# Performance work log

Hardware: AMD Instinct MI355X
Metric: run time of the kernel (lower is better)

## Reference

```python
import jax, jax.numpy as jnp
import numpy as np

NUM_NODES = 1_000_000
H_DIM = 64
OUT_DIM = 32
NUM_RELS = 64
NUM_BASES = 4
N_SRC0 = 400_000
N_DST1 = 100_000
N_DST2 = 20_000
E1 = 600_000
E2 = 300_000


def setup_inputs() -> dict:
    key = jax.random.key(0)
    ks = jax.random.split(key, 16)
    inp = {
        "input_nodes": jax.random.randint(ks[0], (N_SRC0,), 0, NUM_NODES),
        "src1": jax.random.randint(ks[1], (E1,), 0, N_SRC0),
        "dst1": jax.random.randint(ks[2], (E1,), 0, N_DST1),
        "etype1": jax.random.randint(ks[3], (E1,), 0, NUM_RELS),
        "norm1": jax.random.uniform(ks[4], (E1, 1), dtype=jnp.float32),
        "src2": jax.random.randint(ks[5], (E2,), 0, N_DST1),
        "dst2": jax.random.randint(ks[6], (E2,), 0, N_DST2),
        "etype2": jax.random.randint(ks[7], (E2,), 0, NUM_RELS),
        "norm2": jax.random.uniform(ks[8], (E2, 1), dtype=jnp.float32),
        # learned parameters
        "emb": jax.random.normal(ks[9], (NUM_NODES, H_DIM), dtype=jnp.float32),
        "V1": jax.random.normal(ks[10], (NUM_BASES, H_DIM, H_DIM), dtype=jnp.float32) * 0.05,
        "comp1": jax.random.normal(ks[11], (NUM_RELS, NUM_BASES), dtype=jnp.float32) * 0.3,
        "b1": jnp.zeros((H_DIM,), dtype=jnp.float32),
        "V2": jax.random.normal(ks[12], (NUM_BASES, H_DIM, OUT_DIM), dtype=jnp.float32) * 0.05,
        "comp2": jax.random.normal(ks[13], (NUM_RELS, NUM_BASES), dtype=jnp.float32) * 0.3,
        "b2": jnp.zeros((OUT_DIM,), dtype=jnp.float32),
    }
    return inp


def rel_graph_conv(x, src, dst, etype, norm, V, comp, bias, n_dst):
    """Basis-decomposed RelGraphConv (no self-loop): m_e = (x[src_e] @ W_{etype_e}) * norm_e,
    with W_r = sum_b comp[r,b] V[b]; aggregate by sum into dst nodes, then add bias."""
    xe = x[src]                                 # [E, d] gather of source features
    coeff = comp[etype]                         # [E, B] relation coefficients per edge
    y = jnp.einsum('ed,bdo->ebo', xe, V)        # [E, B, o] feature x each basis
    m = jnp.einsum('ebo,eb->eo', y, coeff)      # [E, o] relation-specific message
    m = m * norm                                # per-edge normalization ([E,1] broadcast)
    h = jax.ops.segment_sum(m, dst, num_segments=n_dst)  # scatter-add to dst
    return h + bias


def reference(input_nodes, src1, dst1, etype1, norm1, src2, dst2, etype2, norm2,
              emb, V1, comp1, b1, V2, comp2, b2):
    x = emb[input_nodes]                                           # [N_src0, h]
    h = rel_graph_conv(x, src1, dst1, etype1, norm1, V1, comp1, b1, N_DST1)
    h = jax.nn.relu(h)
    out = rel_graph_conv(h, src2, dst2, etype2, norm2, V2, comp2, b2, N_DST2)
    return out
```

## Files before the change

### kernel.cpp

```cpp
#include <hip/hip_runtime.h>
#include <stdint.h>

#define NUM_NODES 1000000
#define H_DIM 64
#define OUT_DIM 32
#define NUM_RELS 64
#define NUM_BASES 4
#define N_SRC0 400000
#define N_DST1 100000
#define N_DST2 20000
#define E1 600000
#define E2 300000
#define NDST_TOT (N_DST1 + N_DST2)
#define E_TOT (E1 + E2)

typedef __attribute__((ext_vector_type(8))) short bf16x8;
typedef __attribute__((ext_vector_type(4))) float floatx4;

__device__ __forceinline__ unsigned short f2bf(float f){
  union{float f; unsigned u;} v; v.f=f;
  unsigned u=v.u;
  unsigned r=(u + 0x7FFFu + ((u>>16)&1u))>>16;
  return (unsigned short)r;
}
__device__ __forceinline__ float bf2f(unsigned short h){
  union{unsigned u; float f;} v; v.u=((unsigned)h)<<16; return v.f;
}

__global__ void k_init(const float* __restrict__ V1, const float* __restrict__ V2,
                       ushort* __restrict__ Btab1, ushort* __restrict__ Btab2,
                       int* __restrict__ deg){
  int t = blockIdx.x*blockDim.x + threadIdx.x;
  if (t < NDST_TOT) deg[t] = 0;
  if (t < 16384){
    int j = t & 7, lane = (t>>3)&63, kk = (t>>9)&7, nt = t>>12;
    int kdim = kk*32 + (lane>>4)*8 + j;
    int o = nt*16 + (lane&15);
    int k = kdim>>2, b = kdim&3;
    Btab1[t] = f2bf(V1[(b*64 + k)*64 + o]);
  } else if (t < 24576){
    int u = t - 16384;
    int j = u & 7, lane = (u>>3)&63, kk = (u>>9)&7, nt = u>>12;
    int kdim = kk*32 + (lane>>4)*8 + j;
    int o = nt*16 + (lane&15);
    int k = kdim>>2, b = kdim&3;
    Btab2[u] = f2bf(V2[(b*64 + k)*32 + o]);
  }
}

__global__ void k_gather_x(const int* __restrict__ input_nodes,
                           const float* __restrict__ emb,
                           ushort* __restrict__ x_bf){
  int t = blockIdx.x*blockDim.x + threadIdx.x;
  if (t >= N_SRC0*16) return;
  int row = t >> 4, seg = t & 15;
  int idx = input_nodes[row];
  float4 v = ((const float4*)emb)[(size_t)idx*16 + seg];
  ushort4 o; o.x=f2bf(v.x); o.y=f2bf(v.y); o.z=f2bf(v.z); o.w=f2bf(v.w);
  ((ushort4*)x_bf)[(size_t)row*16 + seg] = o;
}

__global__ void k_hist(const int* __restrict__ dst1, const int* __restrict__ dst2,
                       int* __restrict__ deg){
  int t = blockIdx.x*blockDim.x + threadIdx.x;
  if (t < E1) atomicAdd(&deg[dst1[t]], 1);
  else if (t < E_TOT) atomicAdd(&deg[N_DST1 + dst2[t - E1]], 1);
}

__global__ void k_scan_sum(const int* __restrict__ deg, int* __restrict__ bsum, int n){
  __shared__ int lds[256];
  int tid = threadIdx.x;
  int base = blockIdx.x*1024 + tid*4;
  int s = 0;
  #pragma unroll
  for (int j=0;j<4;j++){ int i = base+j; if (i<n) s += deg[i]; }
  lds[tid] = s; __syncthreads();
  for (int off=128; off>0; off>>=1){ if (tid<off) lds[tid] += lds[tid+off]; __syncthreads(); }
  if (tid==0) bsum[blockIdx.x] = lds[0];
}

__global__ void k_scan_bsum(const int* __restrict__ bsum, int* __restrict__ boff, int nb){
  __shared__ int lds[256];
  int tid = threadIdx.x;
  int v = (tid<nb) ? bsum[tid] : 0;
  lds[tid] = v; __syncthreads();
  for (int off=1; off<256; off<<=1){
    int t = (tid>=off) ? lds[tid-off] : 0; __syncthreads();
    lds[tid] += t; __syncthreads();
  }
  if (tid<nb) boff[tid] = lds[tid] - v;
}

__global__ void k_scan_final(const int* __restrict__ deg, const int* __restrict__ boff,
                             int* __restrict__ offs, int* __restrict__ cursor, int n){
  __shared__ int lds[256];
  int tid = threadIdx.x;
  int base = blockIdx.x*1024 + tid*4;
  int a[4]; int s = 0;
  #pragma unroll
  for (int j=0;j<4;j++){ int i = base+j; a[j] = (i<n)?deg[i]:0; s += a[j]; }
  lds[tid] = s; __syncthreads();
  for (int off=1; off<256; off<<=1){
    int t = (tid>=off) ? lds[tid-off] : 0; __syncthreads();
    lds[tid] += t; __syncthreads();
  }
  int run = boff[blockIdx.x] + (lds[tid] - s);
  #pragma unroll
  for (int j=0;j<4;j++){
    int i = base+j;
    if (i<n){
      offs[i] = run; cursor[i] = run;
      run += a[j];
      if (i == n-1) offs[n] = run;
    }
  }
}

__global__ void k_scatter(const int* __restrict__ src1, const int* __restrict__ dst1,
                          const int* __restrict__ ety1, const float* __restrict__ nrm1,
                          const float* __restrict__ comp1,
                          const int* __restrict__ src2, const int* __restrict__ dst2,
                          const int* __restrict__ ety2, const float* __restrict__ nrm2,
                          const float* __restrict__ comp2,
                          int* __restrict__ cursor, int* __restrict__ ssrc,
                          float4* __restrict__ sc){
  int t = blockIdx.x*blockDim.x + threadIdx.x;
  int d, s, et; float nv; const float* comp;
  if (t < E1){
    d = dst1[t]; s = src1[t]; et = ety1[t]; nv = nrm1[t]; comp = comp1;
  } else if (t < E_TOT){
    int e = t - E1;
    d = N_DST1 + dst2[e]; s = src2[e]; et = ety2[e]; nv = nrm2[e]; comp = comp2;
  } else return;
  int p = atomicAdd(&cursor[d], 1);
  ssrc[p] = s;
  float4 cp = ((const float4*)comp)[et];
  float4 c; c.x = cp.x*nv; c.y = cp.y*nv; c.z = cp.z*nv; c.w = cp.w*nv;
  sc[p] = c;
}

__device__ __forceinline__ void agg_rows(const ushort* __restrict__ xin,
                                         const int* __restrict__ offs,
                                         const int* __restrict__ ssrc,
                                         const float4* __restrict__ sc,
                                         int mbase, int w, int lane,
                                         ushort zt[16][264]){
  for (int j = 0; j < 4; j++){
    int row = w*4 + j;
    int d = mbase + row;
    int e0 = offs[d], e1 = offs[d+1];
    float a0=0.f, a1=0.f, a2=0.f, a3=0.f;
    for (int base = e0; base < e1; base += 64){
      int m = e1 - base; if (m > 64) m = 64;
      int se = 0; float4 ce = {0.f,0.f,0.f,0.f};
      if (lane < m){ se = ssrc[base + lane]; ce = sc[base + lane]; }
      for (int i = 0; i < m; i++){
        int s = __shfl(se, i);
        float cx = __shfl(ce.x, i), cy = __shfl(ce.y, i);
        float cz = __shfl(ce.z, i), cw = __shfl(ce.w, i);
        float xv = bf2f(xin[(size_t)s*64 + lane]);
        a0 = fmaf(cx, xv, a0); a1 = fmaf(cy, xv, a1);
        a2 = fmaf(cz, xv, a2); a3 = fmaf(cw, xv, a3);
      }
    }
    ushort4 o; o.x=f2bf(a0); o.y=f2bf(a1); o.z=f2bf(a2); o.w=f2bf(a3);
    *(ushort4*)&zt[row][lane*4] = o;
  }
}

__global__ __launch_bounds__(256) void k_agg_gemm1(
    const ushort* __restrict__ xin, const int* __restrict__ offs,
    const int* __restrict__ ssrc, const float4* __restrict__ sc,
    const ushort* __restrict__ Btab, const float* __restrict__ bias,
    ushort* __restrict__ h_bf){
  __shared__ ushort zt[16][264];
  int lane = threadIdx.x & 63;
  int w = threadIdx.x >> 6;
  int mbase = blockIdx.x * 16;
  agg_rows(xin, offs, ssrc, sc, mbase, w, lane, zt);
  __syncthreads();
  int quad = lane>>4, l15 = lane&15;
  bf16x8 a[8];
  #pragma unroll
  for (int kk=0; kk<8; kk++)
    a[kk] = *(const bf16x8*)&zt[l15][kk*32 + quad*8];
  floatx4 acc = {0.f,0.f,0.f,0.f};
  #pragma unroll
  for (int kk=0; kk<8; kk++){
    bf16x8 b = *((const bf16x8*)(Btab + ((w*8 + kk)*64 + lane)*8));
    acc = __builtin_amdgcn_mfma_f32_16x16x32_bf16(a[kk], b, acc, 0, 0, 0);
  }
  int col = w*16 + l15;
  float bv = bias[col];
  #pragma unroll
  for (int r=0; r<4; r++){
    int row = mbase + quad*4 + r;
    float v = fmaxf(acc[r] + bv, 0.f);
    h_bf[(size_t)row*64 + col] = f2bf(v);
  }
}

__global__ __launch_bounds__(256) void k_agg_gemm2(
    const ushort* __restrict__ xin, const int* __restrict__ offs,
    const int* __restrict__ ssrc, const float4* __restrict__ sc,
    const ushort* __restrict__ Btab, const float* __restrict__ bias,
    float* __restrict__ out){
  __shared__ ushort zt[16][264];
  int lane = threadIdx.x & 63;
  int w = threadIdx.x >> 6;
  int mbase = blockIdx.x * 16;
  agg_rows(xin, offs, ssrc, sc, mbase, w, lane, zt);
  __syncthreads();
  if (w >= 2) return;
  int quad = lane>>4, l15 = lane&15;
  bf16x8 a[8];
  #pragma unroll
  for (int kk=0; kk<8; kk++)
    a[kk] = *(const bf16x8*)&zt[l15][kk*32 + quad*8];
  floatx4 acc = {0.f,0.f,0.f,0.f};
  #pragma unroll
  for (int kk=0; kk<8; kk++){
    bf16x8 b = *((const bf16x8*)(Btab + ((w*8 + kk)*64 + lane)*8));
    acc = __builtin_amdgcn_mfma_f32_16x16x32_bf16(a[kk], b, acc, 0, 0, 0);
  }
  int col = w*16 + l15;
  float bv = bias[col];
  #pragma unroll
  for (int r=0; r<4; r++){
    int row = mbase + quad*4 + r;
    out[(size_t)row*32 + col] = acc[r] + bv;
  }
}

extern "C" void kernel_launch(void* const* d_in, const int* in_sizes, int n_in,
                              void* d_out, int out_size, void* d_ws, size_t ws_size,
                              hipStream_t stream){
  const int*   input_nodes = (const int*)  d_in[0];
  const int*   src1  = (const int*)  d_in[1];
  const int*   dst1  = (const int*)  d_in[2];
  const int*   ety1  = (const int*)  d_in[3];
  const float* norm1 = (const float*)d_in[4];
  const int*   src2  = (const int*)  d_in[5];
  const int*   dst2  = (const int*)  d_in[6];
  const int*   ety2  = (const int*)  d_in[7];
  const float* norm2 = (const float*)d_in[8];
  const float* emb   = (const float*)d_in[9];
  const float* V1    = (const float*)d_in[10];
  const float* comp1 = (const float*)d_in[11];
  const float* b1    = (const float*)d_in[12];
  const float* V2    = (const float*)d_in[13];
  const float* comp2 = (const float*)d_in[14];
  const float* b2    = (const float*)d_in[15];
  float* out = (float*)d_out;

  char* p = (char*)d_ws;
  auto alloc = [&](size_t bytes)->char*{
    char* r = p; p += (bytes + 255) & ~(size_t)255; return r;
  };
  ushort* x_bf  = (ushort*)alloc((size_t)N_SRC0*64*2);
  ushort* h_bf  = (ushort*)alloc((size_t)N_DST1*64*2);
  ushort* Btab1 = (ushort*)alloc(16384*2);
  ushort* Btab2 = (ushort*)alloc(8192*2);
  int* deg  = (int*)alloc((size_t)NDST_TOT*4);
  int* cur  = (int*)alloc((size_t)NDST_TOT*4);
  int* offs = (int*)alloc((size_t)(NDST_TOT+1)*4);
  int* bs   = (int*)alloc(256*4);
  int* bo   = (int*)alloc(256*4);
  int* ssrc = (int*)alloc((size_t)E_TOT*4);
  float4* sc = (float4*)alloc((size_t)E_TOT*16);

  k_init<<<(NDST_TOT + 255)/256, 256, 0, stream>>>(V1, V2, Btab1, Btab2, deg);
  k_gather_x<<<(N_SRC0*16 + 255)/256, 256, 0, stream>>>(input_nodes, emb, x_bf);
  k_hist<<<(E_TOT + 255)/256, 256, 0, stream>>>(dst1, dst2, deg);
  int nb = (NDST_TOT + 1023)/1024;
  k_scan_sum<<<nb, 256, 0, stream>>>(deg, bs, NDST_TOT);
  k_scan_bsum<<<1, 256, 0, stream>>>(bs, bo, nb);
  k_scan_final<<<nb, 256, 0, stream>>>(deg, bo, offs, cur, NDST_TOT);
  k_scatter<<<(E_TOT + 255)/256, 256, 0, stream>>>(src1, dst1, ety1, norm1, comp1,
                                                   src2, dst2, ety2, norm2, comp2,
                                                   cur, ssrc, sc);
  k_agg_gemm1<<<N_DST1/16, 256, 0, stream>>>(x_bf, offs, ssrc, sc, Btab1, b1, h_bf);
  k_agg_gemm2<<<N_DST2/16, 256, 0, stream>>>(h_bf, offs + N_DST1, ssrc, sc, Btab2, b2, out);

  (void)in_sizes; (void)n_in; (void)out_size; (void)ws_size;
}
```

Before: 541.6 us.

## Drop embedding pre-gather; compose input_nodes into edge sources and read emb directly

Removes the kernel that materialized a bf16 copy of all 400k gathered embedding rows. The scatter kernel now maps each layer-1 edge source through input_nodes, and the layer-1 aggregation reads fp32 emb rows directly. This avoids writing and rereading the x buffer, most of whose rows are never touched by edges, at the cost of reading fp32 rows (twice the bytes per edge) at random locations in a 256MB table. The inner edge loop is also unrolled by two so two row loads are in flight at once.

```diff
diff --git a/kernel.cpp b/kernel.cpp
--- a/kernel.cpp
+++ b/kernel.cpp
@@ -48,18 +48,6 @@
   }
 }
 
-__global__ void k_gather_x(const int* __restrict__ input_nodes,
-                           const float* __restrict__ emb,
-                           ushort* __restrict__ x_bf){
-  int t = blockIdx.x*blockDim.x + threadIdx.x;
-  if (t >= N_SRC0*16) return;
-  int row = t >> 4, seg = t & 15;
-  int idx = input_nodes[row];
-  float4 v = ((const float4*)emb)[(size_t)idx*16 + seg];
-  ushort4 o; o.x=f2bf(v.x); o.y=f2bf(v.y); o.z=f2bf(v.z); o.w=f2bf(v.w);
-  ((ushort4*)x_bf)[(size_t)row*16 + seg] = o;
-}
-
 __global__ void k_hist(const int* __restrict__ dst1, const int* __restrict__ dst2,
                        int* __restrict__ deg){
   int t = blockIdx.x*blockDim.x + threadIdx.x;
@@ -116,7 +104,8 @@
   }
 }
 
-__global__ void k_scatter(const int* __restrict__ src1, const int* __restrict__ dst1,
+__global__ void k_scatter(const int* __restrict__ input_nodes,
+                          const int* __restrict__ src1, const int* __restrict__ dst1,
                           const int* __restrict__ ety1, const float* __restrict__ nrm1,
                           const float* __restrict__ comp1,
                           const int* __restrict__ src2, const int* __restrict__ dst2,
@@ -127,7 +116,7 @@
   int t = blockIdx.x*blockDim.x + threadIdx.x;
   int d, s, et; float nv; const float* comp;
   if (t < E1){
-    d = dst1[t]; s = src1[t]; et = ety1[t]; nv = nrm1[t]; comp = comp1;
+    d = dst1[t]; s = input_nodes[src1[t]]; et = ety1[t]; nv = nrm1[t]; comp = comp1;
   } else if (t < E_TOT){
     int e = t - E1;
     d = N_DST1 + dst2[e]; s = src2[e]; et = ety2[e]; nv = nrm2[e]; comp = comp2;
@@ -139,12 +128,16 @@
   sc[p] = c;
 }
 
-__device__ __forceinline__ void agg_rows(const ushort* __restrict__ xin,
-                                         const int* __restrict__ offs,
-                                         const int* __restrict__ ssrc,
-                                         const float4* __restrict__ sc,
-                                         int mbase, int w, int lane,
-                                         ushort zt[16][264]){
+
+__global__ __launch_bounds__(256) void k_agg_gemm1(
+    const float* __restrict__ emb, const int* __restrict__ offs,
+    const int* __restrict__ ssrc, const float4* __restrict__ sc,
+    const ushort* __restrict__ Btab, const float* __restrict__ bias,
+    ushort* __restrict__ h_bf){
+  __shared__ ushort zt[16][264];
+  int lane = threadIdx.x & 63;
+  int w = threadIdx.x >> 6;
+  int mbase = blockIdx.x * 16;
   for (int j = 0; j < 4; j++){
     int row = w*4 + j;
     int d = mbase + row;
@@ -154,30 +147,29 @@
       int m = e1 - base; if (m > 64) m = 64;
       int se = 0; float4 ce = {0.f,0.f,0.f,0.f};
       if (lane < m){ se = ssrc[base + lane]; ce = sc[base + lane]; }
-      for (int i = 0; i < m; i++){
-        int s = __shfl(se, i);
-        float cx = __shfl(ce.x, i), cy = __shfl(ce.y, i);
-        float cz = __shfl(ce.z, i), cw = __shfl(ce.w, i);
-        float xv = bf2f(xin[(size_t)s*64 + lane]);
-        a0 = fmaf(cx, xv, a0); a1 = fmaf(cy, xv, a1);
-        a2 = fmaf(cz, xv, a2); a3 = fmaf(cw, xv, a3);
+      int i = 0;
+      for (; i + 1 < m; i += 2){
+        int s0 = __shfl(se, i), s1 = __shfl(se, i+1);
+        float xv0 = emb[(size_t)s0*64 + lane];
+        float xv1 = emb[(size_t)s1*64 + lane];
+        float c0x=__shfl(ce.x,i), c0y=__shfl(ce.y,i), c0z=__shfl(ce.z,i), c0w=__shfl(ce.w,i);
+        float c1x=__shfl(ce.x,i+1), c1y=__shfl(ce.y,i+1), c1z=__shfl(ce.z,i+1), c1w=__shfl(ce.w,i+1);
+        a0 = fmaf(c0x, xv0, a0); a1 = fmaf(c0y, xv0, a1);
+        a2 = fmaf(c0z, xv0, a2); a3 = fmaf(c0w, xv0, a3);
+        a0 = fmaf(c1x, xv1, a0); a1 = fmaf(c1y, xv1, a1);
+        a2 = fmaf(c1z, xv1, a2); a3 = fmaf(c1w, xv1, a3);
+      }
+      if (i < m){
+        int s0 = __shfl(se, i);
+        float xv0 = emb[(size_t)s0*64 + lane];
+        float c0x=__shfl(ce.x,i), c0y=__shfl(ce.y,i), c0z=__shfl(ce.z,i), c0w=__shfl(ce.w,i);
+        a0 = fmaf(c0x, xv0, a0); a1 = fmaf(c0y, xv0, a1);
+        a2 = fmaf(c0z, xv0, a2); a3 = fmaf(c0w, xv0, a3);
       }
     }
     ushort4 o; o.x=f2bf(a0); o.y=f2bf(a1); o.z=f2bf(a2); o.w=f2bf(a3);
     *(ushort4*)&zt[row][lane*4] = o;
   }
-}
-
-__global__ __launch_bounds__(256) void k_agg_gemm1(
-    const ushort* __restrict__ xin, const int* __restrict__ offs,
-    const int* __restrict__ ssrc, const float4* __restrict__ sc,
-    const ushort* __restrict__ Btab, const float* __restrict__ bias,
-    ushort* __restrict__ h_bf){
-  __shared__ ushort zt[16][264];
-  int lane = threadIdx.x & 63;
-  int w = threadIdx.x >> 6;
-  int mbase = blockIdx.x * 16;
-  agg_rows(xin, offs, ssrc, sc, mbase, w, lane, zt);
   __syncthreads();
   int quad = lane>>4, l15 = lane&15;
   bf16x8 a[8];
@@ -201,7 +193,7 @@
 }
 
 __global__ __launch_bounds__(256) void k_agg_gemm2(
-    const ushort* __restrict__ xin, const int* __restrict__ offs,
+    const ushort* __restrict__ hin, const int* __restrict__ offs,
     const int* __restrict__ ssrc, const float4* __restrict__ sc,
     const ushort* __restrict__ Btab, const float* __restrict__ bias,
     float* __restrict__ out){
@@ -209,7 +201,38 @@
   int lane = threadIdx.x & 63;
   int w = threadIdx.x >> 6;
   int mbase = blockIdx.x * 16;
-  agg_rows(xin, offs, ssrc, sc, mbase, w, lane, zt);
+  for (int j = 0; j < 4; j++){
+    int row = w*4 + j;
+    int d = mbase + row;
+    int e0 = offs[d], e1 = offs[d+1];
+    float a0=0.f, a1=0.f, a2=0.f, a3=0.f;
+    for (int base = e0; base < e1; base += 64){
+      int m = e1 - base; if (m > 64) m = 64;
+      int se = 0; float4 ce = {0.f,0.f,0.f,0.f};
+      if (lane < m){ se = ssrc[base + lane]; ce = sc[base + lane]; }
+      int i = 0;
+      for (; i + 1 < m; i += 2){
+        int s0 = __shfl(se, i), s1 = __shfl(se, i+1);
+        float xv0 = bf2f(hin[(size_t)s0*64 + lane]);
+        float xv1 = bf2f(hin[(size_t)s1*64 + lane]);
+        float c0x=__shfl(ce.x,i), c0y=__shfl(ce.y,i), c0z=__shfl(ce.z,i), c0w=__shfl(ce.w,i);
+        float c1x=__shfl(ce.x,i+1), c1y=__shfl(ce.y,i+1), c1z=__shfl(ce.z,i+1), c1w=__shfl(ce.w,i+1);
+        a0 = fmaf(c0x, xv0, a0); a1 = fmaf(c0y, xv0, a1);
+        a2 = fmaf(c0z, xv0, a2); a3 = fmaf(c0w, xv0, a3);
+        a0 = fmaf(c1x, xv1, a0); a1 = fmaf(c1y, xv1, a1);
+        a2 = fmaf(c1z, xv1, a2); a3 = fmaf(c1w, xv1, a3);
+      }
+      if (i < m){
+        int s0 = __shfl(se, i);
+        float xv0 = bf2f(hin[(size_t)s0*64 + lane]);
+        float c0x=__shfl(ce.x,i), c0y=__shfl(ce.y,i), c0z=__shfl(ce.z,i), c0w=__shfl(ce.w,i);
+        a0 = fmaf(c0x, xv0, a0); a1 = fmaf(c0y, xv0, a1);
+        a2 = fmaf(c0z, xv0, a2); a3 = fmaf(c0w, xv0, a3);
+      }
+    }
+    ushort4 o; o.x=f2bf(a0); o.y=f2bf(a1); o.z=f2bf(a2); o.w=f2bf(a3);
+    *(ushort4*)&zt[row][lane*4] = o;
+  }
   __syncthreads();
   if (w >= 2) return;
   int quad = lane>>4, l15 = lane&15;
@@ -257,7 +280,6 @@
   auto alloc = [&](size_t bytes)->char*{
     char* r = p; p += (bytes + 255) & ~(size_t)255; return r;
   };
-  ushort* x_bf  = (ushort*)alloc((size_t)N_SRC0*64*2);
   ushort* h_bf  = (ushort*)alloc((size_t)N_DST1*64*2);
   ushort* Btab1 = (ushort*)alloc(16384*2);
   ushort* Btab2 = (ushort*)alloc(8192*2);
@@ -270,16 +292,16 @@
   float4* sc = (float4*)alloc((size_t)E_TOT*16);
 
   k_init<<<(NDST_TOT + 255)/256, 256, 0, stream>>>(V1, V2, Btab1, Btab2, deg);
-  k_gather_x<<<(N_SRC0*16 + 255)/256, 256, 0, stream>>>(input_nodes, emb, x_bf);
   k_hist<<<(E_TOT + 255)/256, 256, 0, stream>>>(dst1, dst2, deg);
   int nb = (NDST_TOT + 1023)/1024;
   k_scan_sum<<<nb, 256, 0, stream>>>(deg, bs, NDST_TOT);
   k_scan_bsum<<<1, 256, 0, stream>>>(bs, bo, nb);
   k_scan_final<<<nb, 256, 0, stream>>>(deg, bo, offs, cur, NDST_TOT);
-  k_scatter<<<(E_TOT + 255)/256, 256, 0, stream>>>(src1, dst1, ety1, norm1, comp1,
+  k_scatter<<<(E_TOT + 255)/256, 256, 0, stream>>>(input_nodes,
+                                                   src1, dst1, ety1, norm1, comp1,
                                                    src2, dst2, ety2, norm2, comp2,
                                                    cur, ssrc, sc);
-  k_agg_gemm1<<<N_DST1/16, 256, 0, stream>>>(x_bf, offs, ssrc, sc, Btab1, b1, h_bf);
+  k_agg_gemm1<<<N_DST1/16, 256, 0, stream>>>(emb, offs, ssrc, sc, Btab1, b1, h_bf);
   k_agg_gemm2<<<N_DST2/16, 256, 0, stream>>>(h_bf, offs + N_DST1, ssrc, sc, Btab2, b2, out);
 
   (void)in_sizes; (void)n_in; (void)out_size; (void)ws_size;
```

Measured after the change: 495.1 us. -8.6%, faster.

## Fuse embedding gather into layer-1 aggregation and use one wave per row

Applied to the files above, without the earlier changes.

Drops the separate embedding gather/bf16 conversion kernel and instead remaps layer-1 edge sources through input_nodes during the CSR scatter, so aggregation reads fp32 embedding rows directly. Aggregation kernels now use 1024-thread blocks with one wave per destination row and a 4-way unrolled edge loop for more outstanding loads. This removes a large intermediate write/read but doubles bytes per gathered row and keeps layer-1 inputs in fp32.

```diff
diff --git a/kernel.cpp b/kernel.cpp
--- a/kernel.cpp
+++ b/kernel.cpp
@@ -48,18 +48,6 @@
   }
 }
 
-__global__ void k_gather_x(const int* __restrict__ input_nodes,
-                           const float* __restrict__ emb,
-                           ushort* __restrict__ x_bf){
-  int t = blockIdx.x*blockDim.x + threadIdx.x;
-  if (t >= N_SRC0*16) return;
-  int row = t >> 4, seg = t & 15;
-  int idx = input_nodes[row];
-  float4 v = ((const float4*)emb)[(size_t)idx*16 + seg];
-  ushort4 o; o.x=f2bf(v.x); o.y=f2bf(v.y); o.z=f2bf(v.z); o.w=f2bf(v.w);
-  ((ushort4*)x_bf)[(size_t)row*16 + seg] = o;
-}
-
 __global__ void k_hist(const int* __restrict__ dst1, const int* __restrict__ dst2,
                        int* __restrict__ deg){
   int t = blockIdx.x*blockDim.x + threadIdx.x;
@@ -116,7 +104,8 @@
   }
 }
 
-__global__ void k_scatter(const int* __restrict__ src1, const int* __restrict__ dst1,
+__global__ void k_scatter(const int* __restrict__ input_nodes,
+                          const int* __restrict__ src1, const int* __restrict__ dst1,
                           const int* __restrict__ ety1, const float* __restrict__ nrm1,
                           const float* __restrict__ comp1,
                           const int* __restrict__ src2, const int* __restrict__ dst2,
@@ -127,7 +116,7 @@
   int t = blockIdx.x*blockDim.x + threadIdx.x;
   int d, s, et; float nv; const float* comp;
   if (t < E1){
-    d = dst1[t]; s = src1[t]; et = ety1[t]; nv = nrm1[t]; comp = comp1;
+    d = dst1[t]; s = input_nodes[src1[t]]; et = ety1[t]; nv = nrm1[t]; comp = comp1;
   } else if (t < E_TOT){
     int e = t - E1;
     d = N_DST1 + dst2[e]; s = src2[e]; et = ety2[e]; nv = nrm2[e]; comp = comp2;
@@ -139,37 +128,9 @@
   sc[p] = c;
 }
 
-__device__ __forceinline__ void agg_rows(const ushort* __restrict__ xin,
-                                         const int* __restrict__ offs,
-                                         const int* __restrict__ ssrc,
-                                         const float4* __restrict__ sc,
-                                         int mbase, int w, int lane,
-                                         ushort zt[16][264]){
-  for (int j = 0; j < 4; j++){
-    int row = w*4 + j;
-    int d = mbase + row;
-    int e0 = offs[d], e1 = offs[d+1];
-    float a0=0.f, a1=0.f, a2=0.f, a3=0.f;
-    for (int base = e0; base < e1; base += 64){
-      int m = e1 - base; if (m > 64) m = 64;
-      int se = 0; float4 ce = {0.f,0.f,0.f,0.f};
-      if (lane < m){ se = ssrc[base + lane]; ce = sc[base + lane]; }
-      for (int i = 0; i < m; i++){
-        int s = __shfl(se, i);
-        float cx = __shfl(ce.x, i), cy = __shfl(ce.y, i);
-        float cz = __shfl(ce.z, i), cw = __shfl(ce.w, i);
-        float xv = bf2f(xin[(size_t)s*64 + lane]);
-        a0 = fmaf(cx, xv, a0); a1 = fmaf(cy, xv, a1);
-        a2 = fmaf(cz, xv, a2); a3 = fmaf(cw, xv, a3);
-      }
-    }
-    ushort4 o; o.x=f2bf(a0); o.y=f2bf(a1); o.z=f2bf(a2); o.w=f2bf(a3);
-    *(ushort4*)&zt[row][lane*4] = o;
-  }
-}
-
-__global__ __launch_bounds__(256) void k_agg_gemm1(
-    const ushort* __restrict__ xin, const int* __restrict__ offs,
+
+__global__ __launch_bounds__(1024) void k_agg_gemm1(
+    const float* __restrict__ emb, const int* __restrict__ offs,
     const int* __restrict__ ssrc, const float4* __restrict__ sc,
     const ushort* __restrict__ Btab, const float* __restrict__ bias,
     ushort* __restrict__ h_bf){
@@ -177,8 +138,35 @@
   int lane = threadIdx.x & 63;
   int w = threadIdx.x >> 6;
   int mbase = blockIdx.x * 16;
-  agg_rows(xin, offs, ssrc, sc, mbase, w, lane, zt);
+  int d = mbase + w;
+  int e0 = offs[d], e1 = offs[d+1];
+  float a0=0.f, a1=0.f, a2=0.f, a3=0.f;
+  int elast = e1 - 1;
+  for (int e = e0; e < e1; e += 4){
+    int i0 = e,            i1 = min(e+1, elast);
+    int i2 = min(e+2, elast), i3 = min(e+3, elast);
+    int s0 = ssrc[i0], s1 = ssrc[i1], s2 = ssrc[i2], s3 = ssrc[i3];
+    float4 c0 = sc[i0], c1 = sc[i1], c2 = sc[i2], c3 = sc[i3];
+    if (e+1 > elast){ c1.x=0.f;c1.y=0.f;c1.z=0.f;c1.w=0.f; }
+    if (e+2 > elast){ c2.x=0.f;c2.y=0.f;c2.z=0.f;c2.w=0.f; }
+    if (e+3 > elast){ c3.x=0.f;c3.y=0.f;c3.z=0.f;c3.w=0.f; }
+    float x0 = emb[(size_t)s0*64 + lane];
+    float x1 = emb[(size_t)s1*64 + lane];
+    float x2 = emb[(size_t)s2*64 + lane];
+    float x3 = emb[(size_t)s3*64 + lane];
+    a0 = fmaf(c0.x, x0, a0); a1 = fmaf(c0.y, x0, a1);
+    a2 = fmaf(c0.z, x0, a2); a3 = fmaf(c0.w, x0, a3);
+    a0 = fmaf(c1.x, x1, a0); a1 = fmaf(c1.y, x1, a1);
+    a2 = fmaf(c1.z, x1, a2); a3 = fmaf(c1.w, x1, a3);
+    a0 = fmaf(c2.x, x2, a0); a1 = fmaf(c2.y, x2, a1);
+    a2 = fmaf(c2.z, x2, a2); a3 = fmaf(c2.w, x2, a3);
+    a0 = fmaf(c3.x, x3, a0); a1 = fmaf(c3.y, x3, a1);
+    a2 = fmaf(c3.z, x3, a2); a3 = fmaf(c3.w, x3, a3);
+  }
+  ushort4 o; o.x=f2bf(a0); o.y=f2bf(a1); o.z=f2bf(a2); o.w=f2bf(a3);
+  *(ushort4*)&zt[w][lane*4] = o;
   __syncthreads();
+  if (w >= 4) return;
   int quad = lane>>4, l15 = lane&15;
   bf16x8 a[8];
   #pragma unroll
@@ -200,8 +188,8 @@
   }
 }
 
-__global__ __launch_bounds__(256) void k_agg_gemm2(
-    const ushort* __restrict__ xin, const int* __restrict__ offs,
+__global__ __launch_bounds__(1024) void k_agg_gemm2(
+    const ushort* __restrict__ hin, const int* __restrict__ offs,
     const int* __restrict__ ssrc, const float4* __restrict__ sc,
     const ushort* __restrict__ Btab, const float* __restrict__ bias,
     float* __restrict__ out){
@@ -209,7 +197,33 @@
   int lane = threadIdx.x & 63;
   int w = threadIdx.x >> 6;
   int mbase = blockIdx.x * 16;
-  agg_rows(xin, offs, ssrc, sc, mbase, w, lane, zt);
+  int d = mbase + w;
+  int e0 = offs[d], e1 = offs[d+1];
+  float a0=0.f, a1=0.f, a2=0.f, a3=0.f;
+  int elast = e1 - 1;
+  for (int e = e0; e < e1; e += 4){
+    int i0 = e,            i1 = min(e+1, elast);
+    int i2 = min(e+2, elast), i3 = min(e+3, elast);
+    int s0 = ssrc[i0], s1 = ssrc[i1], s2 = ssrc[i2], s3 = ssrc[i3];
+    float4 c0 = sc[i0], c1 = sc[i1], c2 = sc[i2], c3 = sc[i3];
+    if (e+1 > elast){ c1.x=0.f;c1.y=0.f;c1.z=0.f;c1.w=0.f; }
+    if (e+2 > elast){ c2.x=0.f;c2.y=0.f;c2.z=0.f;c2.w=0.f; }
+    if (e+3 > elast){ c3.x=0.f;c3.y=0.f;c3.z=0.f;c3.w=0.f; }
+    float x0 = bf2f(hin[(size_t)s0*64 + lane]);
+    float x1 = bf2f(hin[(size_t)s1*64 + lane]);
+    float x2 = bf2f(hin[(size_t)s2*64 + lane]);
+    float x3 = bf2f(hin[(size_t)s3*64 + lane]);
+    a0 = fmaf(c0.x, x0, a0); a1 = fmaf(c0.y, x0, a1);
+    a2 = fmaf(c0.z, x0, a2); a3 = fmaf(c0.w, x0, a3);
+    a0 = fmaf(c1.x, x1, a0); a1 = fmaf(c1.y, x1, a1);
+    a2 = fmaf(c1.z, x1, a2); a3 = fmaf(c1.w, x1, a3);
+    a0 = fmaf(c2.x, x2, a0); a1 = fmaf(c2.y, x2, a1);
+    a2 = fmaf(c2.z, x2, a2); a3 = fmaf(c2.w, x2, a3);
+    a0 = fmaf(c3.x, x3, a0); a1 = fmaf(c3.y, x3, a1);
+    a2 = fmaf(c3.z, x3, a2); a3 = fmaf(c3.w, x3, a3);
+  }
+  ushort4 o; o.x=f2bf(a0); o.y=f2bf(a1); o.z=f2bf(a2); o.w=f2bf(a3);
+  *(ushort4*)&zt[w][lane*4] = o;
   __syncthreads();
   if (w >= 2) return;
   int quad = lane>>4, l15 = lane&15;
@@ -257,7 +271,6 @@
   auto alloc = [&](size_t bytes)->char*{
     char* r = p; p += (bytes + 255) & ~(size_t)255; return r;
   };
-  ushort* x_bf  = (ushort*)alloc((size_t)N_SRC0*64*2);
   ushort* h_bf  = (ushort*)alloc((size_t)N_DST1*64*2);
   ushort* Btab1 = (ushort*)alloc(16384*2);
   ushort* Btab2 = (ushort*)alloc(8192*2);
@@ -270,17 +283,17 @@
   float4* sc = (float4*)alloc((size_t)E_TOT*16);
 
   k_init<<<(NDST_TOT + 255)/256, 256, 0, stream>>>(V1, V2, Btab1, Btab2, deg);
-  k_gather_x<<<(N_SRC0*16 + 255)/256, 256, 0, stream>>>(input_nodes, emb, x_bf);
   k_hist<<<(E_TOT + 255)/256, 256, 0, stream>>>(dst1, dst2, deg);
   int nb = (NDST_TOT + 1023)/1024;
   k_scan_sum<<<nb, 256, 0, stream>>>(deg, bs, NDST_TOT);
   k_scan_bsum<<<1, 256, 0, stream>>>(bs, bo, nb);
   k_scan_final<<<nb, 256, 0, stream>>>(deg, bo, offs, cur, NDST_TOT);
-  k_scatter<<<(E_TOT + 255)/256, 256, 0, stream>>>(src1, dst1, ety1, norm1, comp1,
+  k_scatter<<<(E_TOT + 255)/256, 256, 0, stream>>>(input_nodes,
+                                                   src1, dst1, ety1, norm1, comp1,
                                                    src2, dst2, ety2, norm2, comp2,
                                                    cur, ssrc, sc);
-  k_agg_gemm1<<<N_DST1/16, 256, 0, stream>>>(x_bf, offs, ssrc, sc, Btab1, b1, h_bf);
-  k_agg_gemm2<<<N_DST2/16, 256, 0, stream>>>(h_bf, offs + N_DST1, ssrc, sc, Btab2, b2, out);
+  k_agg_gemm1<<<N_DST1/16, 1024, 0, stream>>>(emb, offs, ssrc, sc, Btab1, b1, h_bf);
+  k_agg_gemm2<<<N_DST2/16, 1024, 0, stream>>>(h_bf, offs + N_DST1, ssrc, sc, Btab2, b2, out);
 
   (void)in_sizes; (void)n_in; (void)out_size; (void)ws_size;
 }
```

After: 506.9 us. 6.4% less time.
